# Kernel tuning notes

Hardware: AMD Instinct MI355X
Metric: run time of the kernel (lower is better)

The kernel has to match this reference:

```python
import jax, jax.numpy as jnp
import numpy as np

Z_CH, TEXT_DIM, HID = 3, 512, 64
B, H, W = 16, 256, 256


def setup_inputs() -> dict:
    key = jax.random.key(0)
    ks = jax.random.split(key, 8)
    z = jax.random.normal(ks[0], (B, Z_CH, H, W), dtype=jnp.float32)
    text_vec = jax.random.normal(ks[1], (B, TEXT_DIM), dtype=jnp.float32)
    # 1x1 conv == per-pixel linear: store weights as [out, in]
    z_proj_w = jax.random.normal(ks[2], (HID, Z_CH), dtype=jnp.float32) * (1.0 / np.sqrt(Z_CH))
    z_proj_b = jnp.zeros((HID,), dtype=jnp.float32)
    text_proj_w = jax.random.normal(ks[3], (HID, TEXT_DIM), dtype=jnp.float32) * (1.0 / np.sqrt(TEXT_DIM))
    text_proj_b = jnp.zeros((HID,), dtype=jnp.float32)
    out_w = jax.random.normal(ks[4], (Z_CH, HID), dtype=jnp.float32) * (1.0 / np.sqrt(HID))
    out_b = jnp.zeros((Z_CH,), dtype=jnp.float32)
    log_gamma = jnp.asarray(1.0 / HID, dtype=jnp.float32)
    alpha = jnp.asarray(0.5, dtype=jnp.float32)
    c = jnp.asarray(1.0, dtype=jnp.float32)
    w = jnp.ones((3,), dtype=jnp.float32)
    return {"z": z, "text_vec": text_vec, "z_proj_w": z_proj_w, "z_proj_b": z_proj_b,
            "text_proj_w": text_proj_w, "text_proj_b": text_proj_b,
            "out_w": out_w, "out_b": out_b,
            "log_gamma": log_gamma, "alpha": alpha, "c": c, "w": w}


def reference(z, text_vec, z_proj_w, z_proj_b, text_proj_w, text_proj_b,
              out_w, out_b, log_gamma, alpha, c, w):
    # z_proj: 1x1 conv -> [B, HID, H, W]
    z_map = jnp.einsum('bchw,oc->bohw', z, z_proj_w) + z_proj_b[None, :, None, None]
    # text_proj: [B, HID]
    t = text_vec @ text_proj_w.T + text_proj_b
    # MultiKernel diagonal: k(z_i, t) per pixel. t_seq broadcasts the same
    # vector to all HW positions, so diag of the full [HW,HW] kernel matrix
    # equals the per-pixel kernel between z_map pixel and t.
    gamma = jnp.exp(log_gamma)
    diff = z_map - t[:, :, None, None]            # [B, HID, H, W]
    dist = jnp.sum(diff * diff, axis=1)            # squared euclidean, [B, H, W]
    k_lin = jnp.einsum('bchw,bc->bhw', z_map, t)   # [B, H, W]
    k_rbf = jnp.exp(-gamma * dist)
    k_poly = (alpha * k_lin + c) ** 2
    k = (w[0] * k_rbf + w[1] * k_lin + w[2] * k_poly) / (jnp.sum(w) + 1e-8)
    weight = k[:, None, :, :]                       # [B, 1, H, W]
    z_fused = z_map * (1.0 + jax.nn.sigmoid(weight))
    out = jnp.einsum('bchw,oc->bohw', z_fused, out_w) + out_b[None, :, None, None]
    return out
```

## Files before the change

### kernel.cpp

```cpp
#include <hip/hip_runtime.h>
#include <math.h>

#define HW_PIX 65536
#define HID_N 64
#define TDIM 512
#define NBATCH 16

__device__ __forceinline__ float wred64(float v) {
#pragma unroll
    for (int off = 32; off > 0; off >>= 1) v += __shfl_xor(v, off, 64);
    return v;
}

__global__ __launch_bounds__(256) void prep_kernel(
    const float* __restrict__ text_vec,
    const float* __restrict__ text_proj_w,
    const float* __restrict__ text_proj_b,
    const float* __restrict__ z_proj_w,
    const float* __restrict__ z_proj_b,
    const float* __restrict__ out_w,
    float* __restrict__ ws)
{
    const int b   = blockIdx.x;
    const int tid = threadIdx.x;
    const int o   = tid >> 2;
    const int q   = tid & 3;

    const float4* tv   = (const float4*)(text_vec + (size_t)b * TDIM);
    const float4* wrow = (const float4*)(text_proj_w + (size_t)o * TDIM);

    float acc = 0.f;
#pragma unroll 8
    for (int i = q * 32; i < q * 32 + 32; ++i) {
        float4 a = tv[i];
        float4 w = wrow[i];
        acc = fmaf(a.x, w.x, fmaf(a.y, w.y, fmaf(a.z, w.z, fmaf(a.w, w.w, acc))));
    }
    acc += __shfl_xor(acc, 1, 64);
    acc += __shfl_xor(acc, 2, 64);

    __shared__ float t_sh[HID_N];
    if (q == 0) t_sh[o] = acc + text_proj_b[o];
    __syncthreads();

    if (tid < 64) {
        float t  = t_sh[tid];
        float w0 = z_proj_w[tid * 3 + 0];
        float w1 = z_proj_w[tid * 3 + 1];
        float w2 = z_proj_w[tid * 3 + 2];
        float zb = z_proj_b[tid];

        float u0 = wred64(w0 * t);
        float u1 = wred64(w1 * t);
        float u2 = wred64(w2 * t);
        float s  = wred64(zb * t);
        float tn = wred64(t * t);
        if (tid == 0) {
            float* pb = ws + b * 8;
            pb[0] = u0; pb[1] = u1; pb[2] = u2; pb[3] = s; pb[4] = tn;
        }

        if (b == 0) {
            float o0 = out_w[0 * 64 + tid];
            float o1 = out_w[1 * 64 + tid];
            float o2 = out_w[2 * 64 + tid];
            float G00 = wred64(w0 * w0), G01 = wred64(w0 * w1), G02 = wred64(w0 * w2);
            float G11 = wred64(w1 * w1), G12 = wred64(w1 * w2), G22 = wred64(w2 * w2);
            float M00 = wred64(o0 * w0), M01 = wred64(o0 * w1), M02 = wred64(o0 * w2);
            float M10 = wred64(o1 * w0), M11 = wred64(o1 * w1), M12 = wred64(o1 * w2);
            float M20 = wred64(o2 * w0), M21 = wred64(o2 * w1), M22 = wred64(o2 * w2);
            float v0  = wred64(o0 * zb), v1  = wred64(o1 * zb), v2  = wred64(o2 * zb);
            float g0  = wred64(w0 * zb), g1  = wred64(w1 * zb), g2  = wred64(w2 * zb);
            float bn  = wred64(zb * zb);
            if (tid == 0) {
                float* c = ws + 128;
                c[0] = G00; c[1] = G01; c[2] = G02; c[3] = G11; c[4] = G12; c[5] = G22;
                c[6] = M00; c[7] = M01; c[8] = M02;
                c[9] = M10; c[10] = M11; c[11] = M12;
                c[12] = M20; c[13] = M21; c[14] = M22;
                c[15] = v0; c[16] = v1; c[17] = v2;
                c[18] = g0; c[19] = g1; c[20] = g2;
                c[21] = bn;
            }
        }
    }
}

__global__ __launch_bounds__(256) void fuse_kernel(
    const float* __restrict__ z,
    const float* __restrict__ out_bias,
    const float* __restrict__ log_gamma,
    const float* __restrict__ alpha_p,
    const float* __restrict__ c_p,
    const float* __restrict__ wv,
    const float* __restrict__ ws,
    float* __restrict__ out)
{
    const int blk = blockIdx.x;
    const int b   = blk >> 6;
    const int p   = ((blk & 63) << 10) + (threadIdx.x << 2);

    const float* C = ws + 128;
    const float G00 = C[0], G01 = C[1], G02 = C[2], G11 = C[3], G12 = C[4], G22 = C[5];
    const float M00 = C[6], M01 = C[7], M02 = C[8];
    const float M10 = C[9], M11 = C[10], M12 = C[11];
    const float M20 = C[12], M21 = C[13], M22 = C[14];
    const float v0 = C[15], v1 = C[16], v2 = C[17];
    const float g0 = C[18], g1 = C[19], g2 = C[20], bn = C[21];

    const float* pb = ws + b * 8;
    const float u0 = pb[0], u1 = pb[1], u2 = pb[2], s = pb[3], tn = pb[4];

    const float gamma = __expf(log_gamma[0]);
    const float alpha = alpha_p[0], cc = c_p[0];
    const float w0 = wv[0], w1 = wv[1], w2 = wv[2];
    const float invw = 1.0f / (w0 + w1 + w2 + 1e-8f);
    const float ob0 = out_bias[0], ob1 = out_bias[1], ob2 = out_bias[2];

    const float e0 = g0 - u0, e1 = g1 - u1, e2 = g2 - u2;
    const float d0 = bn - 2.f * s + tn;

    const float* zb = z + (size_t)b * 3 * HW_PIX + p;
    float4 q0 = *(const float4*)(zb);
    float4 q1 = *(const float4*)(zb + HW_PIX);
    float4 q2 = *(const float4*)(zb + 2 * HW_PIX);

    float X[4] = {q0.x, q0.y, q0.z, q0.w};
    float Y[4] = {q1.x, q1.y, q1.z, q1.w};
    float Z[4] = {q2.x, q2.y, q2.z, q2.w};
    float O0[4], O1[4], O2[4];

#pragma unroll
    for (int j = 0; j < 4; ++j) {
        const float x = X[j], y = Y[j], zc = Z[j];
        const float klin = fmaf(x, u0, fmaf(y, u1, fmaf(zc, u2, s)));
        const float quad = x * fmaf(2.f, fmaf(G01, y, G02 * zc), G00 * x)
                         + y * fmaf(2.f, G12 * zc, G11 * y)
                         + G22 * zc * zc;
        const float dist = quad + 2.f * fmaf(e0, x, fmaf(e1, y, e2 * zc)) + d0;
        const float krbf = __expf(-gamma * dist);
        float kp = fmaf(alpha, klin, cc);
        kp = kp * kp;
        const float k = (w0 * krbf + w1 * klin + w2 * kp) * invw;
        const float sig = 1.f / (1.f + __expf(-k));
        const float scale = 1.f + sig;

        const float m0 = fmaf(M00, x, fmaf(M01, y, fmaf(M02, zc, v0)));
        const float m1 = fmaf(M10, x, fmaf(M11, y, fmaf(M12, zc, v1)));
        const float m2 = fmaf(M20, x, fmaf(M21, y, fmaf(M22, zc, v2)));
        O0[j] = fmaf(scale, m0, ob0);
        O1[j] = fmaf(scale, m1, ob1);
        O2[j] = fmaf(scale, m2, ob2);
    }

    float* ob = out + (size_t)b * 3 * HW_PIX + p;
    *(float4*)(ob)              = make_float4(O0[0], O0[1], O0[2], O0[3]);
    *(float4*)(ob + HW_PIX)     = make_float4(O1[0], O1[1], O1[2], O1[3]);
    *(float4*)(ob + 2 * HW_PIX) = make_float4(O2[0], O2[1], O2[2], O2[3]);
}

extern "C" void kernel_launch(void* const* d_in, const int* in_sizes, int n_in,
                              void* d_out, int out_size, void* d_ws, size_t ws_size,
                              hipStream_t stream) {
    const float* z           = (const float*)d_in[0];
    const float* text_vec    = (const float*)d_in[1];
    const float* z_proj_w    = (const float*)d_in[2];
    const float* z_proj_b    = (const float*)d_in[3];
    const float* text_proj_w = (const float*)d_in[4];
    const float* text_proj_b = (const float*)d_in[5];
    const float* out_w       = (const float*)d_in[6];
    const float* out_b       = (const float*)d_in[7];
    const float* log_gamma   = (const float*)d_in[8];
    const float* alpha       = (const float*)d_in[9];
    const float* c           = (const float*)d_in[10];
    const float* w           = (const float*)d_in[11];
    float* out = (float*)d_out;
    float* ws  = (float*)d_ws;

    prep_kernel<<<NBATCH, 256, 0, stream>>>(text_vec, text_proj_w, text_proj_b,
                                            z_proj_w, z_proj_b, out_w, ws);
    fuse_kernel<<<NBATCH * 64, 256, 0, stream>>>(z, out_b, log_gamma, alpha, c, w,
                                                 ws, out);
}
```

Baseline: 96.53 us.

## Fuse prep and pixel kernels into one launch with per-block recompute

Merges the per-batch text-projection prep kernel into the pixel kernel: every block recomputes the text projection and the Gram and mixing constants in shared memory, with z loads issued first so they overlap that work. Each thread now handles 8 pixels (512 blocks instead of 1024), and loads and stores use nontemporal hints. This removes one kernel launch and the serial dependency between the two launches. In exchange, the redundant 512-length dot products and roughly 30 wave reductions run in every block, and more registers are live per thread.

```diff
diff --git a/kernel.cpp b/kernel.cpp
--- a/kernel.cpp
+++ b/kernel.cpp
@@ -2,9 +2,12 @@
 #include <math.h>
 
 #define HW_PIX 65536
-#define HID_N 64
 #define TDIM 512
 #define NBATCH 16
+#define BLK_PER_B 32
+#define PIX_PER_BLK 2048
+
+typedef float v4f __attribute__((ext_vector_type(4)));
 
 __device__ __forceinline__ float wred64(float v) {
 #pragma unroll
@@ -12,126 +15,111 @@
     return v;
 }
 
-__global__ __launch_bounds__(256) void prep_kernel(
+__global__ __launch_bounds__(256) void fused_all(
+    const float* __restrict__ z,
     const float* __restrict__ text_vec,
+    const float* __restrict__ z_proj_w,
+    const float* __restrict__ z_proj_b,
     const float* __restrict__ text_proj_w,
     const float* __restrict__ text_proj_b,
-    const float* __restrict__ z_proj_w,
-    const float* __restrict__ z_proj_b,
     const float* __restrict__ out_w,
-    float* __restrict__ ws)
+    const float* __restrict__ out_bias,
+    const float* __restrict__ log_gamma,
+    const float* __restrict__ alpha_p,
+    const float* __restrict__ c_p,
+    const float* __restrict__ wv,
+    float* __restrict__ out)
 {
-    const int b   = blockIdx.x;
     const int tid = threadIdx.x;
-    const int o   = tid >> 2;
-    const int q   = tid & 3;
+    const int b   = blockIdx.x >> 5;
+    const int pb  = blockIdx.x & 31;
+    const int p0  = pb * PIX_PER_BLK + tid * 4;
 
-    const float4* tv   = (const float4*)(text_vec + (size_t)b * TDIM);
-    const float4* wrow = (const float4*)(text_proj_w + (size_t)o * TDIM);
+    const float* zbase = z + (size_t)b * 3 * HW_PIX;
+    v4f A0 = __builtin_nontemporal_load((const v4f*)(zbase + p0));
+    v4f A1 = __builtin_nontemporal_load((const v4f*)(zbase + p0 + 1024));
+    v4f B0 = __builtin_nontemporal_load((const v4f*)(zbase + HW_PIX + p0));
+    v4f B1 = __builtin_nontemporal_load((const v4f*)(zbase + HW_PIX + p0 + 1024));
+    v4f C0 = __builtin_nontemporal_load((const v4f*)(zbase + 2 * HW_PIX + p0));
+    v4f C1 = __builtin_nontemporal_load((const v4f*)(zbase + 2 * HW_PIX + p0 + 1024));
+
+    const float gamma = __expf(log_gamma[0]);
+    const float alpha = alpha_p[0], cc = c_p[0];
+    const float kw0 = wv[0], kw1 = wv[1], kw2 = wv[2];
+    const float invw = 1.0f / (kw0 + kw1 + kw2 + 1e-8f);
+    const float ob0 = out_bias[0], ob1 = out_bias[1], ob2 = out_bias[2];
+
+    const int o = tid >> 2;
+    const int q = tid & 3;
+    const float4* tv = (const float4*)(text_vec + (size_t)b * TDIM);
+    const float4* wr = (const float4*)(text_proj_w + (size_t)o * TDIM);
 
     float acc = 0.f;
 #pragma unroll 8
     for (int i = q * 32; i < q * 32 + 32; ++i) {
         float4 a = tv[i];
-        float4 w = wrow[i];
-        acc = fmaf(a.x, w.x, fmaf(a.y, w.y, fmaf(a.z, w.z, fmaf(a.w, w.w, acc))));
+        float4 ww = wr[i];
+        acc = fmaf(a.x, ww.x, fmaf(a.y, ww.y, fmaf(a.z, ww.z, fmaf(a.w, ww.w, acc))));
     }
     acc += __shfl_xor(acc, 1, 64);
     acc += __shfl_xor(acc, 2, 64);
 
-    __shared__ float t_sh[HID_N];
+    __shared__ float t_sh[64];
+    __shared__ float c_sh[32];
     if (q == 0) t_sh[o] = acc + text_proj_b[o];
     __syncthreads();
 
     if (tid < 64) {
-        float t  = t_sh[tid];
-        float w0 = z_proj_w[tid * 3 + 0];
-        float w1 = z_proj_w[tid * 3 + 1];
-        float w2 = z_proj_w[tid * 3 + 2];
-        float zb = z_proj_b[tid];
+        const float t  = t_sh[tid];
+        const float w0 = z_proj_w[tid * 3 + 0];
+        const float w1 = z_proj_w[tid * 3 + 1];
+        const float w2 = z_proj_w[tid * 3 + 2];
+        const float zb = z_proj_b[tid];
+        const float o0 = out_w[0 * 64 + tid];
+        const float o1 = out_w[1 * 64 + tid];
+        const float o2 = out_w[2 * 64 + tid];
 
-        float u0 = wred64(w0 * t);
-        float u1 = wred64(w1 * t);
-        float u2 = wred64(w2 * t);
-        float s  = wred64(zb * t);
-        float tn = wred64(t * t);
+        float u0 = wred64(w0 * t),  u1 = wred64(w1 * t),  u2 = wred64(w2 * t);
+        float s  = wred64(zb * t),  tn = wred64(t * t);
+        float G00 = wred64(w0 * w0), G01 = wred64(w0 * w1), G02 = wred64(w0 * w2);
+        float G11 = wred64(w1 * w1), G12 = wred64(w1 * w2), G22 = wred64(w2 * w2);
+        float M00 = wred64(o0 * w0), M01 = wred64(o0 * w1), M02 = wred64(o0 * w2);
+        float M10 = wred64(o1 * w0), M11 = wred64(o1 * w1), M12 = wred64(o1 * w2);
+        float M20 = wred64(o2 * w0), M21 = wred64(o2 * w1), M22 = wred64(o2 * w2);
+        float v0  = wred64(o0 * zb), v1  = wred64(o1 * zb), v2  = wred64(o2 * zb);
+        float g0  = wred64(w0 * zb), g1  = wred64(w1 * zb), g2  = wred64(w2 * zb);
+        float bn  = wred64(zb * zb);
         if (tid == 0) {
-            float* pb = ws + b * 8;
-            pb[0] = u0; pb[1] = u1; pb[2] = u2; pb[3] = s; pb[4] = tn;
-        }
-
-        if (b == 0) {
-            float o0 = out_w[0 * 64 + tid];
-            float o1 = out_w[1 * 64 + tid];
-            float o2 = out_w[2 * 64 + tid];
-            float G00 = wred64(w0 * w0), G01 = wred64(w0 * w1), G02 = wred64(w0 * w2);
-            float G11 = wred64(w1 * w1), G12 = wred64(w1 * w2), G22 = wred64(w2 * w2);
-            float M00 = wred64(o0 * w0), M01 = wred64(o0 * w1), M02 = wred64(o0 * w2);
-            float M10 = wred64(o1 * w0), M11 = wred64(o1 * w1), M12 = wred64(o1 * w2);
-            float M20 = wred64(o2 * w0), M21 = wred64(o2 * w1), M22 = wred64(o2 * w2);
-            float v0  = wred64(o0 * zb), v1  = wred64(o1 * zb), v2  = wred64(o2 * zb);
-            float g0  = wred64(w0 * zb), g1  = wred64(w1 * zb), g2  = wred64(w2 * zb);
-            float bn  = wred64(zb * zb);
-            if (tid == 0) {
-                float* c = ws + 128;
-                c[0] = G00; c[1] = G01; c[2] = G02; c[3] = G11; c[4] = G12; c[5] = G22;
-                c[6] = M00; c[7] = M01; c[8] = M02;
-                c[9] = M10; c[10] = M11; c[11] = M12;
-                c[12] = M20; c[13] = M21; c[14] = M22;
-                c[15] = v0; c[16] = v1; c[17] = v2;
-                c[18] = g0; c[19] = g1; c[20] = g2;
-                c[21] = bn;
-            }
+            c_sh[0] = u0;  c_sh[1] = u1;  c_sh[2] = u2;  c_sh[3] = s;   c_sh[4] = tn;
+            c_sh[5] = G00; c_sh[6] = G01; c_sh[7] = G02; c_sh[8] = G11; c_sh[9] = G12; c_sh[10] = G22;
+            c_sh[11] = M00; c_sh[12] = M01; c_sh[13] = M02;
+            c_sh[14] = M10; c_sh[15] = M11; c_sh[16] = M12;
+            c_sh[17] = M20; c_sh[18] = M21; c_sh[19] = M22;
+            c_sh[20] = v0;  c_sh[21] = v1;  c_sh[22] = v2;
+            c_sh[23] = g0;  c_sh[24] = g1;  c_sh[25] = g2;
+            c_sh[26] = bn;
         }
     }
-}
+    __syncthreads();
 
-__global__ __launch_bounds__(256) void fuse_kernel(
-    const float* __restrict__ z,
-    const float* __restrict__ out_bias,
-    const float* __restrict__ log_gamma,
-    const float* __restrict__ alpha_p,
-    const float* __restrict__ c_p,
-    const float* __restrict__ wv,
-    const float* __restrict__ ws,
-    float* __restrict__ out)
-{
-    const int blk = blockIdx.x;
-    const int b   = blk >> 6;
-    const int p   = ((blk & 63) << 10) + (threadIdx.x << 2);
-
-    const float* C = ws + 128;
-    const float G00 = C[0], G01 = C[1], G02 = C[2], G11 = C[3], G12 = C[4], G22 = C[5];
-    const float M00 = C[6], M01 = C[7], M02 = C[8];
-    const float M10 = C[9], M11 = C[10], M12 = C[11];
-    const float M20 = C[12], M21 = C[13], M22 = C[14];
-    const float v0 = C[15], v1 = C[16], v2 = C[17];
-    const float g0 = C[18], g1 = C[19], g2 = C[20], bn = C[21];
-
-    const float* pb = ws + b * 8;
-    const float u0 = pb[0], u1 = pb[1], u2 = pb[2], s = pb[3], tn = pb[4];
-
-    const float gamma = __expf(log_gamma[0]);
-    const float alpha = alpha_p[0], cc = c_p[0];
-    const float w0 = wv[0], w1 = wv[1], w2 = wv[2];
-    const float invw = 1.0f / (w0 + w1 + w2 + 1e-8f);
-    const float ob0 = out_bias[0], ob1 = out_bias[1], ob2 = out_bias[2];
+    const float u0 = c_sh[0], u1 = c_sh[1], u2 = c_sh[2], s = c_sh[3], tn = c_sh[4];
+    const float G00 = c_sh[5], G01 = c_sh[6], G02 = c_sh[7], G11 = c_sh[8], G12 = c_sh[9], G22 = c_sh[10];
+    const float M00 = c_sh[11], M01 = c_sh[12], M02 = c_sh[13];
+    const float M10 = c_sh[14], M11 = c_sh[15], M12 = c_sh[16];
+    const float M20 = c_sh[17], M21 = c_sh[18], M22 = c_sh[19];
+    const float v0 = c_sh[20], v1 = c_sh[21], v2 = c_sh[22];
+    const float g0 = c_sh[23], g1 = c_sh[24], g2 = c_sh[25], bn = c_sh[26];
 
     const float e0 = g0 - u0, e1 = g1 - u1, e2 = g2 - u2;
     const float d0 = bn - 2.f * s + tn;
 
-    const float* zb = z + (size_t)b * 3 * HW_PIX + p;
-    float4 q0 = *(const float4*)(zb);
-    float4 q1 = *(const float4*)(zb + HW_PIX);
-    float4 q2 = *(const float4*)(zb + 2 * HW_PIX);
-
-    float X[4] = {q0.x, q0.y, q0.z, q0.w};
-    float Y[4] = {q1.x, q1.y, q1.z, q1.w};
-    float Z[4] = {q2.x, q2.y, q2.z, q2.w};
-    float O0[4], O1[4], O2[4];
+    float X[8] = {A0.x, A0.y, A0.z, A0.w, A1.x, A1.y, A1.z, A1.w};
+    float Y[8] = {B0.x, B0.y, B0.z, B0.w, B1.x, B1.y, B1.z, B1.w};
+    float Z[8] = {C0.x, C0.y, C0.z, C0.w, C1.x, C1.y, C1.z, C1.w};
+    float O0[8], O1[8], O2[8];
 
 #pragma unroll
-    for (int j = 0; j < 4; ++j) {
+    for (int j = 0; j < 8; ++j) {
         const float x = X[j], y = Y[j], zc = Z[j];
         const float klin = fmaf(x, u0, fmaf(y, u1, fmaf(zc, u2, s)));
         const float quad = x * fmaf(2.f, fmaf(G01, y, G02 * zc), G00 * x)
@@ -141,7 +129,7 @@
         const float krbf = __expf(-gamma * dist);
         float kp = fmaf(alpha, klin, cc);
         kp = kp * kp;
-        const float k = (w0 * krbf + w1 * klin + w2 * kp) * invw;
+        const float k = (kw0 * krbf + kw1 * klin + kw2 * kp) * invw;
         const float sig = 1.f / (1.f + __expf(-k));
         const float scale = 1.f + sig;
 
@@ -153,10 +141,20 @@
         O2[j] = fmaf(scale, m2, ob2);
     }
 
-    float* ob = out + (size_t)b * 3 * HW_PIX + p;
-    *(float4*)(ob)              = make_float4(O0[0], O0[1], O0[2], O0[3]);
-    *(float4*)(ob + HW_PIX)     = make_float4(O1[0], O1[1], O1[2], O1[3]);
-    *(float4*)(ob + 2 * HW_PIX) = make_float4(O2[0], O2[1], O2[2], O2[3]);
+    float* obase = out + (size_t)b * 3 * HW_PIX;
+    v4f R;
+    R.x = O0[0]; R.y = O0[1]; R.z = O0[2]; R.w = O0[3];
+    __builtin_nontemporal_store(R, (v4f*)(obase + p0));
+    R.x = O0[4]; R.y = O0[5]; R.z = O0[6]; R.w = O0[7];
+    __builtin_nontemporal_store(R, (v4f*)(obase + p0 + 1024));
+    R.x = O1[0]; R.y = O1[1]; R.z = O1[2]; R.w = O1[3];
+    __builtin_nontemporal_store(R, (v4f*)(obase + HW_PIX + p0));
+    R.x = O1[4]; R.y = O1[5]; R.z = O1[6]; R.w = O1[7];
+    __builtin_nontemporal_store(R, (v4f*)(obase + HW_PIX + p0 + 1024));
+    R.x = O2[0]; R.y = O2[1]; R.z = O2[2]; R.w = O2[3];
+    __builtin_nontemporal_store(R, (v4f*)(obase + 2 * HW_PIX + p0));
+    R.x = O2[4]; R.y = O2[5]; R.z = O2[6]; R.w = O2[7];
+    __builtin_nontemporal_store(R, (v4f*)(obase + 2 * HW_PIX + p0 + 1024));
 }
 
 extern "C" void kernel_launch(void* const* d_in, const int* in_sizes, int n_in,
@@ -175,10 +173,8 @@
     const float* c           = (const float*)d_in[10];
     const float* w           = (const float*)d_in[11];
     float* out = (float*)d_out;
-    float* ws  = (float*)d_ws;
 
-    prep_kernel<<<NBATCH, 256, 0, stream>>>(text_vec, text_proj_w, text_proj_b,
-                                            z_proj_w, z_proj_b, out_w, ws);
-    fuse_kernel<<<NBATCH * 64, 256, 0, stream>>>(z, out_b, log_gamma, alpha, c, w,
-                                                 ws, out);
+    fused_all<<<NBATCH * BLK_PER_B, 256, 0, stream>>>(
+        z, text_vec, z_proj_w, z_proj_b, text_proj_w, text_proj_b,
+        out_w, out_b, log_gamma, alpha, c, w, out);
 }
```

After: 102.2 us. +5.9%, slower.
